# Optimization experiments

Hardware: AMD Instinct MI355X
Metric: run time of the kernel (lower is better)

## Reference

```python
import jax, jax.numpy as jnp
import numpy as np

B, N, D = 8, 9856, 256
HEADS = 8
WH, WW = 7, 11
HID = 512  # int(D * 2.0)
EPS = 1e-5


def layernorm(x, g, b):
    mu = jnp.mean(x, axis=-1, keepdims=True)
    var = jnp.mean(jnp.square(x - mu), axis=-1, keepdims=True)
    return (x - mu) * jax.lax.rsqrt(var + EPS) * g + b


def setup_inputs() -> dict:
    key = jax.random.key(0)
    ks = jax.random.split(key, 6)
    s = lambda k, shape: (jax.random.normal(k, shape, jnp.float32) * 0.02)
    return {
        "x": jax.random.normal(ks[0], (B, N, D), jnp.float32),
        "norm1_g": jnp.ones((D,), jnp.float32),
        "norm1_b": jnp.zeros((D,), jnp.float32),
        "in_proj_w": s(ks[1], (3 * D, D)),
        "in_proj_b": jnp.zeros((3 * D,), jnp.float32),
        "out_w": s(ks[2], (D, D)),
        "out_b": jnp.zeros((D,), jnp.float32),
        "norm2_g": jnp.ones((D,), jnp.float32),
        "norm2_b": jnp.zeros((D,), jnp.float32),
        "fc1_w": s(ks[3], (HID, D)),
        "fc1_b": jnp.zeros((HID,), jnp.float32),
        "fc2_w": s(ks[4], (D, HID)),
        "fc2_b": jnp.zeros((D,), jnp.float32),
        "h": 56,
        "w": 176,
    }


def reference(x, norm1_g, norm1_b, in_proj_w, in_proj_b, out_w, out_b,
              norm2_g, norm2_b, fc1_w, fc1_b, fc2_w, fc2_b, h, w):
    Bx, Nx, Dx = x.shape
    n_h, n_w = h // WH, w // WW  # chosen dims divide evenly -> pad_h = pad_w = 0
    hd = Dx // HEADS
    L = WH * WW  # 77 tokens per window

    res = x
    xn = layernorm(x, norm1_g, norm1_b)

    # window partition: (B, h*w, D) -> (B*n_h*n_w, wh*ww, D)
    win = xn.reshape(Bx, n_h, WH, n_w, WW, Dx)
    win = win.transpose(0, 1, 3, 2, 4, 5).reshape(-1, L, Dx)

    # MultiheadAttention (batch_first) on each window independently
    qkv = win @ in_proj_w.T + in_proj_b          # (NW, L, 3D)
    q, k, v = jnp.split(qkv, 3, axis=-1)
    NW = win.shape[0]
    q = q.reshape(NW, L, HEADS, hd).transpose(0, 2, 1, 3)
    k = k.reshape(NW, L, HEADS, hd).transpose(0, 2, 1, 3)
    v = v.reshape(NW, L, HEADS, hd).transpose(0, 2, 1, 3)
    scores = jnp.einsum("nhld,nhmd->nhlm", q, k) / jnp.sqrt(jnp.float32(hd))
    attn = jax.nn.softmax(scores, axis=-1)
    o = jnp.einsum("nhlm,nhmd->nhld", attn, v)   # (NW, H, L, hd)
    o = o.transpose(0, 2, 1, 3).reshape(NW, L, Dx)
    o = o @ out_w.T + out_b

    # window reverse: (B*n_h*n_w, wh*ww, D) -> (B, h*w, D)
    o = o.reshape(Bx, n_h, n_w, WH, WW, Dx)
    o = o.transpose(0, 1, 3, 2, 4, 5).reshape(Bx, Nx, Dx)

    x = res + o
    res = x
    xn2 = layernorm(x, norm2_g, norm2_b)
    hmid = jax.nn.gelu(xn2 @ fc1_w.T + fc1_b, approximate=False)
    mlp = hmid @ fc2_w.T + fc2_b
    return res + mlp
```

## Files before the change

### kernel.cpp

```cpp
#include <hip/hip_runtime.h>
#include <hip/hip_bf16.h>

typedef unsigned short u16;
typedef unsigned int   u32;

typedef __bf16 bf16x8 __attribute__((ext_vector_type(8)));
typedef float  f32x4  __attribute__((ext_vector_type(4)));

__device__ __forceinline__ u16 f2bf(float f) {
  u32 u = __float_as_uint(f);
  u += 0x7fffu + ((u >> 16) & 1u);
  return (u16)(u >> 16);
}
__device__ __forceinline__ u32 pack2(float a, float b) {
  return (u32)f2bf(a) | ((u32)f2bf(b) << 16);
}
__device__ __forceinline__ void gld16(const void* g, void* l) {
  __builtin_amdgcn_global_load_lds(
      (const __attribute__((address_space(1))) unsigned int*)g,
      (__attribute__((address_space(3))) unsigned int*)l, 16, 0, 0);
}

#define TOK_M   78848
#define DIM     256
#define NWIN    1024
#define WINL    77

template<int K, int NF>
__device__ __forceinline__ void cvt_chunk(const float* __restrict__ src,
                                          u16* __restrict__ dst, int rel)
{
  constexpr int KT = K / 32;
  constexpr int PN = NF * 16;
  const int lane  = rel & 63;
  const int g     = rel >> 6;
  const int nf    = g % NF;
  const int kt    = (g / NF) % KT;
  const int panel = g / (NF * KT);
  const int col   = panel * PN + nf * 16 + (lane & 15);
  const int k0    = kt * 32 + (lane >> 4) * 8;
  const float4 a = *(const float4*)(src + (size_t)col * K + k0);
  const float4 b = *(const float4*)(src + (size_t)col * K + k0 + 4);
  uint4 o;
  o.x = pack2(a.x, a.y); o.y = pack2(a.z, a.w);
  o.z = pack2(b.x, b.y); o.w = pack2(b.z, b.w);
  *(uint4*)(dst + (size_t)rel * 8) = o;
}
__device__ __forceinline__ void cvt_plain(const float* __restrict__ src,
                                          u16* __restrict__ dst, int rel)
{
  const int i = rel * 8;
  const float4 a = *(const float4*)(src + i);
  const float4 b = *(const float4*)(src + i + 4);
  uint4 o;
  o.x = pack2(a.x, a.y); o.y = pack2(a.z, a.w);
  o.z = pack2(b.x, b.y); o.w = pack2(b.z, b.w);
  *(uint4*)(dst + i) = o;
}

__global__ __launch_bounds__(256)
void cvt_w(const float* __restrict__ wqkv, const float* __restrict__ wout,
           const float* __restrict__ w1, const float* __restrict__ w2,
           u16* __restrict__ out)
{
  const int c = blockIdx.x * 256 + threadIdx.x;
  if      (c < 24576) cvt_chunk<256, 8>(wqkv, out,          c);
  else if (c < 32768) cvt_plain(wout, out + 196608, c - 24576);
  else if (c < 49152) cvt_chunk<256, 8>(w1,   out + 262144, c - 32768);
  else                cvt_plain(w2,   out + 393216, c - 49152);
}

template<int NPAN, int EPI, int OBF, int PERM>
__global__ __launch_bounds__(256, 2)
void lngemm(const float* __restrict__ X, const u16* __restrict__ Wimg,
            const float* __restrict__ lg, const float* __restrict__ lb,
            const float* __restrict__ bias, void* __restrict__ Cout)
{
  constexpr int K  = 256;
  constexpr int KT = K / 32;
  constexpr int N  = NPAN * 128;
  constexpr int NSTEP = NPAN * KT;
  __shared__ u16 At[64 * K];
  __shared__ u16 Bs[4][4096];

  const int tid  = threadIdx.x;
  const int wave = tid >> 6, lane = tid & 63;
  const int quad = lane >> 4, l16 = lane & 15;
  const int wy = wave >> 1, wx = wave & 1;
  const int rowbase = blockIdx.x * 64;

  {
    const float4 gg = *(const float4*)(lg + lane * 4);
    const float4 bb = *(const float4*)(lb + lane * 4);
    const int c = lane * 4;
    float4 xv[16];
#pragma unroll
    for (int r = 0; r < 16; ++r)
      xv[r] = *(const float4*)(X + (size_t)(rowbase + wave * 16 + r) * 256 + c);
#pragma unroll
    for (int r = 0; r < 16; ++r) {
      const int row = wave * 16 + r;
      const float4 v = xv[r];
      float s = v.x + v.y + v.z + v.w;
#pragma unroll
      for (int off = 32; off; off >>= 1) s += __shfl_xor(s, off);
      const float mu = s * (1.f / 256.f);
      const float dx = v.x - mu, dy = v.y - mu, dz = v.z - mu, dw = v.w - mu;
      float q = dx * dx + dy * dy + dz * dz + dw * dw;
#pragma unroll
      for (int off = 32; off; off >>= 1) q += __shfl_xor(q, off);
      const float rstd = rsqrtf(q * (1.f / 256.f) + 1e-5f);
      uint2 o;
      o.x = pack2(dx * rstd * gg.x + bb.x, dy * rstd * gg.y + bb.y);
      o.y = pack2(dz * rstd * gg.z + bb.z, dw * rstd * gg.w + bb.w);
      *(uint2*)(At + row * 256 + (c ^ ((row & 7) * 8))) = o;
    }
  }
  gld16(Wimg + tid * 8,        Bs[0] + tid * 8);
  gld16(Wimg + 2048 + tid * 8, Bs[0] + 2048 + tid * 8);
  gld16(Wimg + 4096 + tid * 8,        Bs[1] + tid * 8);
  gld16(Wimg + 4096 + 2048 + tid * 8, Bs[1] + 2048 + tid * 8);

  int step = 0;
  for (int np = 0; np < NPAN; ++np) {
    f32x4 acc[2][4];
#pragma unroll
    for (int mi = 0; mi < 2; ++mi)
#pragma unroll
      for (int ni = 0; ni < 4; ++ni) {
        f32x4 z = {0.f, 0.f, 0.f, 0.f};
        acc[mi][ni] = z;
      }
#pragma unroll
    for (int kt = 0; kt < KT; ++kt, ++step) {
      {
        const int sn = (step + 2 < NSTEP) ? step + 2 : NSTEP - 1;
        const u16* src = Wimg + (size_t)sn * 4096;
        u16* dst = Bs[(step + 2) & 3];
        gld16(src + tid * 8,        dst + tid * 8);
        gld16(src + 2048 + tid * 8, dst + 2048 + tid * 8);
      }
      asm volatile("s_waitcnt vmcnt(4) lgkmcnt(0)" ::: "memory");
      __builtin_amdgcn_s_barrier();
      __builtin_amdgcn_sched_barrier(0);
      bf16x8 af[2], bv[4];
#pragma unroll
      for (int mi = 0; mi < 2; ++mi) {
        const int row = wy * 32 + mi * 16 + l16;
        af[mi] = *(const bf16x8*)(At + row * 256 +
                                  ((kt * 32 + quad * 8) ^ ((row & 7) * 8)));
      }
#pragma unroll
      for (int ni = 0; ni < 4; ++ni)
        bv[ni] = *(const bf16x8*)(Bs[step & 3] + ((wx * 4 + ni) * 64 + lane) * 8);
#pragma unroll
      for (int mi = 0; mi < 2; ++mi)
#pragma unroll
        for (int ni = 0; ni < 4; ++ni)
          acc[mi][ni] = __builtin_amdgcn_mfma_f32_16x16x32_bf16(
              af[mi], bv[ni], acc[mi][ni], 0, 0, 0);
    }
    const int col0 = np * 128 + wx * 64 + l16;
#pragma unroll
    for (int mi = 0; mi < 2; ++mi) {
      const int r = rowbase + wy * 32 + mi * 16 + quad * 4;
#pragma unroll
      for (int e = 0; e < 4; ++e) {
        const int gr = r + e;
        size_t orow = (size_t)gr;
        if (PERM) {
          const int b  = gr / 9856, n = gr - b * 9856;
          const int y  = n / 176,  xc = n - y * 176;
          const int ih = y / 7,    rr = y - ih * 7;
          const int iw = xc / 11,  cc = xc - iw * 11;
          orow = (size_t)(((b * 8 + ih) * 16 + iw)) * 77 + rr * 11 + cc;
        }
#pragma unroll
        for (int ni = 0; ni < 4; ++ni) {
          const int col = col0 + ni * 16;
          float v = acc[mi][ni][e] + bias[col];
          if (EPI == 2) v = 0.5f * v * (1.f + erff(v * 0.70710678118654752f));
          const size_t idx = orow * N + col;
          if (OBF) ((u16*)Cout)[idx] = f2bf(v);
          else     ((float*)Cout)[idx] = v;
        }
      }
    }
  }
}

template<int EPI, int OBF>
__global__ __launch_bounds__(256, 2)
void gemm_mfma(const u16* __restrict__ A, const u16* __restrict__ W,
               const float* __restrict__ bias, const float* res,
               void* Cout, int N, int K)
{
  __shared__ u16 As[4][4096];
  __shared__ u16 Bs[4][4096];

  const int tid  = threadIdx.x;
  const int wave = tid >> 6, lane = tid & 63;
  const int wy = wave >> 1, wx = wave & 1;
  const int quad = lane >> 4, l16 = lane & 15;
  const int m0 = blockIdx.y * 128;
  const int n0 = blockIdx.x * 128;

  const int s0 = tid, s1 = tid + 256;
  const int r0 = s0 >> 2, r1 = s1 >> 2;
  const int kb0 = (s0 & 3) ^ ((r0 >> 1) & 3);
  const int kb1 = (s1 & 3) ^ ((r1 >> 1) & 3);
  const u16* Ag0 = A + (size_t)(m0 + r0) * K + kb0 * 8;
  const u16* Ag1 = A + (size_t)(m0 + r1) * K + kb1 * 8;
  const u16* Bg0 = W + (size_t)(n0 + r0) * K + kb0 * 8;
  const u16* Bg1 = W + (size_t)(n0 + r1) * K + kb1 * 8;

  const int kbs = quad ^ ((l16 >> 1) & 3);
  const int aoff = (wy * 64 + l16) * 32 + kbs * 8;
  const int boff = (wx * 64 + l16) * 32 + kbs * 8;

  f32x4 acc[4][4];
#pragma unroll
  for (int i = 0; i < 4; ++i)
#pragma unroll
    for (int j = 0; j < 4; ++j) {
      f32x4 z = {0.f, 0.f, 0.f, 0.f};
      acc[i][j] = z;
    }

  const int NT = K >> 5;
  auto stage = [&](int tile, int buf) {
    const int ko = tile * 32;
    gld16(Ag0 + ko, &As[buf][s0 * 8]);
    gld16(Ag1 + ko, &As[buf][s1 * 8]);
    gld16(Bg0 + ko, &Bs[buf][s0 * 8]);
    gld16(Bg1 + ko, &Bs[buf][s1 * 8]);
  };
  stage(0, 0);
  stage(1, 1);

  for (int t = 0; t < NT; ++t) {
    stage((t + 2 < NT) ? t + 2 : NT - 1, (t + 2) & 3);
    asm volatile("s_waitcnt vmcnt(8) lgkmcnt(0)" ::: "memory");
    __builtin_amdgcn_s_barrier();
    __builtin_amdgcn_sched_barrier(0);
    const u16* Ar = &As[t & 3][aoff];
    const u16* Br = &Bs[t & 3][boff];
    bf16x8 af[4], bv[4];
#pragma unroll
    for (int i = 0; i < 4; ++i) {
      af[i] = *(const bf16x8*)(Ar + i * 16 * 32);
      bv[i] = *(const bf16x8*)(Br + i * 16 * 32);
    }
#pragma unroll
    for (int mi = 0; mi < 4; ++mi)
#pragma unroll
      for (int ni = 0; ni < 4; ++ni)
        acc[mi][ni] = __builtin_amdgcn_mfma_f32_16x16x32_bf16(
            af[mi], bv[ni], acc[mi][ni], 0, 0, 0);
  }

  const int gr0 = m0 + wy * 64 + quad * 4;
  const int gc0 = n0 + wx * 64 + l16;
#pragma unroll
  for (int ni = 0; ni < 4; ++ni) {
    const int gc = gc0 + ni * 16;
    const float bvs = bias[gc];
#pragma unroll
    for (int mi = 0; mi < 4; ++mi) {
      const int gr = gr0 + mi * 16;
      f32x4 a = acc[mi][ni];
#pragma unroll
      for (int e = 0; e < 4; ++e) {
        float v = a[e] + bvs;
        const size_t idx = (size_t)(gr + e) * N + gc;
        if (EPI == 1) v += res[idx];
        else if (EPI == 2) v = 0.5f * v * (1.f + erff(v * 0.70710678118654752f));
        if (OBF) ((u16*)Cout)[idx] = f2bf(v);
        else     ((float*)Cout)[idx] = v;
      }
    }
  }
}

#define PSTR 104
__global__ __launch_bounds__(128)
void attn_mfma(const u16* __restrict__ qkv, u16* __restrict__ onat)
{
  __shared__ __bf16 Pb[2][80 * PSTR];

  const int tid  = threadIdx.x;
  const int wave = tid >> 6, lane = tid & 63;
  const int quad = lane >> 4, l16 = lane & 15;
  const int pair = blockIdx.x * 2 + wave;
  const int nw   = pair >> 3, head = pair & 7;
  const size_t base = (size_t)nw * 77 * 768;
  const int hoff = head * 32;
  __bf16* P = Pb[wave];

  {
    uint4 z = {0, 0, 0, 0};
    for (int r = lane; r < 80; r += 64) {
      *(uint4*)(P + r * PSTR + 80) = z;
      *(uint4*)(P + r * PSTR + 88) = z;
    }
  }

  bf16x8 qf[5], kf[5];
  const u16* qp = qkv + base + hoff + quad * 8;
#pragma unroll
  for (int mi = 0; mi < 5; ++mi) {
    const size_t row = (size_t)(l16 + 16 * mi) * 768;
    qf[mi] = *(const bf16x8*)(qp + row);
    kf[mi] = *(const bf16x8*)(qp + row + 256);
  }

  f32x4 s[5][5];
#pragma unroll
  for (int mi = 0; mi < 5; ++mi)
#pragma unroll
    for (int ni = 0; ni < 5; ++ni) {
      f32x4 z = {0.f, 0.f, 0.f, 0.f};
      s[mi][ni] = z;
    }
#pragma unroll
  for (int mi = 0; mi < 5; ++mi)
#pragma unroll
    for (int ni = 0; ni < 5; ++ni)
      s[mi][ni] = __builtin_amdgcn_mfma_f32_16x16x32_bf16(
          qf[mi], kf[ni], s[mi][ni], 0, 0, 0);

  bf16x8 vf[3][2];
  {
    const __bf16* vbb = (const __bf16*)(qkv + base + 512 + hoff + l16);
#pragma unroll
    for (int ks = 0; ks < 3; ++ks)
#pragma unroll
      for (int ni = 0; ni < 2; ++ni)
#pragma unroll
        for (int jj = 0; jj < 8; ++jj) {
          const int k = ks * 32 + quad * 8 + jj;
          vf[ks][ni][jj] = (k < 77) ? vbb[(size_t)k * 768 + 16 * ni] : (__bf16)0.f;
        }
  }

  if (l16 >= 13) {
#pragma unroll
    for (int mi = 0; mi < 5; ++mi)
#pragma unroll
      for (int e = 0; e < 4; ++e) s[mi][4][e] = -1e30f;
  }

  const float c = 0.17677669529663687f * 1.4426950408889634f;
  float inv[5][4];
#pragma unroll
  for (int mi = 0; mi < 5; ++mi)
#pragma unroll
    for (int e = 0; e < 4; ++e) {
      float mx = s[mi][0][e];
#pragma unroll
      for (int ni = 1; ni < 5; ++ni) mx = fmaxf(mx, s[mi][ni][e]);
#pragma unroll
      for (int off = 1; off < 16; off <<= 1) mx = fmaxf(mx, __shfl_xor(mx, off));
      float sum = 0.f;
#pragma unroll
      for (int ni = 0; ni < 5; ++ni) {
        const float ev = exp2f((s[mi][ni][e] - mx) * c);
        s[mi][ni][e] = ev;
        sum += ev;
      }
#pragma unroll
      for (int off = 1; off < 16; off <<= 1) sum += __shfl_xor(sum, off);
      inv[mi][e] = 1.f / sum;
    }

#pragma unroll
  for (int mi = 0; mi < 5; ++mi)
#pragma unroll
    for (int e = 0; e < 4; ++e) {
      const int m = quad * 4 + e + 16 * mi;
#pragma unroll
      for (int ni = 0; ni < 5; ++ni)
        P[m * PSTR + l16 + 16 * ni] = (__bf16)(s[mi][ni][e] * inv[mi][e]);
    }

  f32x4 o[5][2];
#pragma unroll
  for (int mi = 0; mi < 5; ++mi)
#pragma unroll
    for (int ni = 0; ni < 2; ++ni) {
      f32x4 z = {0.f, 0.f, 0.f, 0.f};
      o[mi][ni] = z;
    }
#pragma unroll
  for (int ks = 0; ks < 3; ++ks)
#pragma unroll
    for (int mi = 0; mi < 5; ++mi) {
      const bf16x8 af = *(const bf16x8*)(P + (l16 + 16 * mi) * PSTR + ks * 32 + quad * 8);
#pragma unroll
      for (int ni = 0; ni < 2; ++ni)
        o[mi][ni] = __builtin_amdgcn_mfma_f32_16x16x32_bf16(
            af, vf[ks][ni], o[mi][ni], 0, 0, 0);
    }

  const int b  = nw >> 7;
  const int ih = (nw >> 4) & 7;
  const int iw = nw & 15;
#pragma unroll
  for (int mi = 0; mi < 5; ++mi)
#pragma unroll
    for (int e = 0; e < 4; ++e) {
      const int t = quad * 4 + e + 16 * mi;
      if (t < 77) {
        const int rr = t / 11, cc = t - rr * 11;
        const int y = ih * 7 + rr, xc = iw * 11 + cc;
        const size_t nat = (size_t)b * 9856 + (size_t)y * 176 + xc;
        u16* dst = onat + nat * DIM + hoff + l16;
        dst[0]  = f2bf(o[mi][0][e]);
        dst[16] = f2bf(o[mi][1][e]);
      }
    }
}

extern "C" void kernel_launch(void* const* d_in, const int* in_sizes, int n_in,
                              void* d_out, int out_size, void* d_ws, size_t ws_size,
                              hipStream_t stream)
{
  (void)in_sizes; (void)n_in; (void)out_size; (void)ws_size;
  const float* x    = (const float*)d_in[0];
  const float* g1   = (const float*)d_in[1];
  const float* b1   = (const float*)d_in[2];
  const float* wqkv = (const float*)d_in[3];
  const float* bqkv = (const float*)d_in[4];
  const float* wout = (const float*)d_in[5];
  const float* bout = (const float*)d_in[6];
  const float* g2   = (const float*)d_in[7];
  const float* b2   = (const float*)d_in[8];
  const float* w1   = (const float*)d_in[9];
  const float* bf1  = (const float*)d_in[10];
  const float* w2   = (const float*)d_in[11];
  const float* bf2  = (const float*)d_in[12];

  char* ws = (char*)d_ws;
  u16*   qkv  = (u16*)(ws);
  u16*   onat = (u16*)(ws + 161480704);
  u16*   wb   = (u16*)(ws + 201850880);
  u16*   wqkv_b = wb;
  u16*   wout_b = wb + 196608;
  u16*   w1_b   = wb + 262144;
  u16*   w2_b   = wb + 393216;
  float* x2   = (float*)d_out;

  cvt_w<<<256, 256, 0, stream>>>(wqkv, wout, w1, w2, wb);
  lngemm<6, 0, 1, 1><<<1232, 256, 0, stream>>>(x, wqkv_b, g1, b1, bqkv, qkv);
  attn_mfma<<<4096, 128, 0, stream>>>(qkv, onat);
  gemm_mfma<1, 0><<<dim3(2, 616), 256, 0, stream>>>(onat, wout_b, bout, x, x2, 256, 256);
  lngemm<4, 2, 1, 0><<<1232, 256, 0, stream>>>(x2, w1_b, g2, b2, bf1, qkv);
  gemm_mfma<1, 0><<<dim3(2, 616), 256, 0, stream>>>(qkv, w2_b, bf2, x2, x2, 256, 512);
}
```

Measured before the change: 582.0 us.

## Fuse out-proj with residual+LN2, keep A fragments in registers across GEMMs

Replaces the generic 128x128 tiled GEMM with row-panel GEMMs that hold each wave's A fragments in registers and stream pre-swizzled weight panels through LDS. The out-projection kernel now also adds the residual and computes LayerNorm2, writing both x2 and a bf16 normalized copy. This removes the separate reread of x2 in the LN-fused fc1 kernel. The QKV kernel reuses one LDS buffer for both the A tile and the B stages, raising occupancy to 3 blocks. Holding A in registers increases register pressure, and per-wave 16-row tiles lower weight reuse per block.

Result: faster. 510.4 us (-12.3%).

```diff
diff --git a/kernel.cpp b/kernel.cpp
--- a/kernel.cpp
+++ b/kernel.cpp
@@ -23,8 +23,6 @@
 
 #define TOK_M   78848
 #define DIM     256
-#define NWIN    1024
-#define WINL    77
 
 template<int K, int NF>
 __device__ __forceinline__ void cvt_chunk(const float* __restrict__ src,
@@ -46,17 +44,6 @@
   o.z = pack2(b.x, b.y); o.w = pack2(b.z, b.w);
   *(uint4*)(dst + (size_t)rel * 8) = o;
 }
-__device__ __forceinline__ void cvt_plain(const float* __restrict__ src,
-                                          u16* __restrict__ dst, int rel)
-{
-  const int i = rel * 8;
-  const float4 a = *(const float4*)(src + i);
-  const float4 b = *(const float4*)(src + i + 4);
-  uint4 o;
-  o.x = pack2(a.x, a.y); o.y = pack2(a.z, a.w);
-  o.z = pack2(b.x, b.y); o.w = pack2(b.z, b.w);
-  *(uint4*)(dst + i) = o;
-}
 
 __global__ __launch_bounds__(256)
 void cvt_w(const float* __restrict__ wqkv, const float* __restrict__ wout,
@@ -65,23 +52,21 @@
 {
   const int c = blockIdx.x * 256 + threadIdx.x;
   if      (c < 24576) cvt_chunk<256, 8>(wqkv, out,          c);
-  else if (c < 32768) cvt_plain(wout, out + 196608, c - 24576);
+  else if (c < 32768) cvt_chunk<256, 8>(wout, out + 196608, c - 24576);
   else if (c < 49152) cvt_chunk<256, 8>(w1,   out + 262144, c - 32768);
-  else                cvt_plain(w2,   out + 393216, c - 49152);
-}
-
-template<int NPAN, int EPI, int OBF, int PERM>
-__global__ __launch_bounds__(256, 2)
-void lngemm(const float* __restrict__ X, const u16* __restrict__ Wimg,
-            const float* __restrict__ lg, const float* __restrict__ lb,
-            const float* __restrict__ bias, void* __restrict__ Cout)
-{
-  constexpr int K  = 256;
-  constexpr int KT = K / 32;
+  else                cvt_chunk<512, 8>(w2,   out + 393216, c - 49152);
+}
+
+template<int NPAN>
+__global__ __launch_bounds__(256, 3)
+void lngemm_qkv(const float* __restrict__ X, const u16* __restrict__ Wimg,
+                const float* __restrict__ lg, const float* __restrict__ lb,
+                const float* __restrict__ bias, u16* __restrict__ Cout)
+{
+  constexpr int KT = 8;
   constexpr int N  = NPAN * 128;
   constexpr int NSTEP = NPAN * KT;
-  __shared__ u16 At[64 * K];
-  __shared__ u16 Bs[4][4096];
+  __shared__ u16 U[16384];
 
   const int tid  = threadIdx.x;
   const int wave = tid >> 6, lane = tid & 63;
@@ -113,13 +98,25 @@
       uint2 o;
       o.x = pack2(dx * rstd * gg.x + bb.x, dy * rstd * gg.y + bb.y);
       o.y = pack2(dz * rstd * gg.z + bb.z, dw * rstd * gg.w + bb.w);
-      *(uint2*)(At + row * 256 + (c ^ ((row & 7) * 8))) = o;
-    }
-  }
-  gld16(Wimg + tid * 8,        Bs[0] + tid * 8);
-  gld16(Wimg + 2048 + tid * 8, Bs[0] + 2048 + tid * 8);
-  gld16(Wimg + 4096 + tid * 8,        Bs[1] + tid * 8);
-  gld16(Wimg + 4096 + 2048 + tid * 8, Bs[1] + 2048 + tid * 8);
+      *(uint2*)(U + row * 256 + (c ^ ((row & 7) * 8))) = o;
+    }
+  }
+  __syncthreads();
+  bf16x8 af[2][8];
+#pragma unroll
+  for (int mi = 0; mi < 2; ++mi) {
+    const int row = wy * 32 + mi * 16 + l16;
+#pragma unroll
+    for (int kt = 0; kt < 8; ++kt)
+      af[mi][kt] = *(const bf16x8*)(U + row * 256 +
+                                    ((kt * 32 + quad * 8) ^ ((row & 7) * 8)));
+  }
+  __syncthreads();
+
+  gld16(Wimg + tid * 8,               U + tid * 8);
+  gld16(Wimg + 2048 + tid * 8,        U + 2048 + tid * 8);
+  gld16(Wimg + 4096 + tid * 8,        U + 4096 + tid * 8);
+  gld16(Wimg + 4096 + 2048 + tid * 8, U + 4096 + 2048 + tid * 8);
 
   int step = 0;
   for (int np = 0; np < NPAN; ++np) {
@@ -131,6 +128,87 @@
         f32x4 z = {0.f, 0.f, 0.f, 0.f};
         acc[mi][ni] = z;
       }
+#pragma unroll
+    for (int kt = 0; kt < KT; ++kt, ++step) {
+      {
+        const int sn = (step + 2 < NSTEP) ? step + 2 : NSTEP - 1;
+        const u16* src = Wimg + (size_t)sn * 4096;
+        u16* dst = U + ((step + 2) & 3) * 4096;
+        gld16(src + tid * 8,        dst + tid * 8);
+        gld16(src + 2048 + tid * 8, dst + 2048 + tid * 8);
+      }
+      asm volatile("s_waitcnt vmcnt(4) lgkmcnt(0)" ::: "memory");
+      __builtin_amdgcn_s_barrier();
+      __builtin_amdgcn_sched_barrier(0);
+      const u16* B0 = U + (step & 3) * 4096;
+      bf16x8 bv[4];
+#pragma unroll
+      for (int ni = 0; ni < 4; ++ni)
+        bv[ni] = *(const bf16x8*)(B0 + ((wx * 4 + ni) * 64 + lane) * 8);
+#pragma unroll
+      for (int mi = 0; mi < 2; ++mi)
+#pragma unroll
+        for (int ni = 0; ni < 4; ++ni)
+          acc[mi][ni] = __builtin_amdgcn_mfma_f32_16x16x32_bf16(
+              af[mi][kt], bv[ni], acc[mi][ni], 0, 0, 0);
+    }
+    const int col0 = np * 128 + wx * 64 + l16;
+#pragma unroll
+    for (int mi = 0; mi < 2; ++mi) {
+      const int r = rowbase + wy * 32 + mi * 16 + quad * 4;
+#pragma unroll
+      for (int e = 0; e < 4; ++e) {
+        const int gr = r + e;
+        const int b  = gr / 9856, n = gr - b * 9856;
+        const int y  = n / 176,  xc = n - y * 176;
+        const int ih = y / 7,    rr = y - ih * 7;
+        const int iw = xc / 11,  cc = xc - iw * 11;
+        const size_t orow = (size_t)(((b * 8 + ih) * 16 + iw)) * 77 + rr * 11 + cc;
+#pragma unroll
+        for (int ni = 0; ni < 4; ++ni) {
+          const int col = col0 + ni * 16;
+          Cout[orow * N + col] = f2bf(acc[mi][ni][e] + bias[col]);
+        }
+      }
+    }
+  }
+}
+
+template<int K, int NPAN, int EPI, int OBF>
+__global__ __launch_bounds__(256, 3)
+void gemmA(const u16* __restrict__ A, const u16* __restrict__ Wimg,
+           const float* __restrict__ bias, const float* __restrict__ res,
+           void* __restrict__ Cout)
+{
+  constexpr int KT = K / 32;
+  constexpr int N  = NPAN * 128;
+  constexpr int NSTEP = NPAN * KT;
+  __shared__ u16 Bs[4][4096];
+
+  const int tid  = threadIdx.x;
+  const int wave = tid >> 6, lane = tid & 63;
+  const int quad = lane >> 4, l16 = lane & 15;
+  const int row0 = blockIdx.x * 64 + wave * 16;
+
+  bf16x8 af[KT];
+  {
+    const u16* Ap = A + (size_t)(row0 + l16) * K + quad * 8;
+#pragma unroll
+    for (int kt = 0; kt < KT; ++kt) af[kt] = *(const bf16x8*)(Ap + kt * 32);
+  }
+  gld16(Wimg + tid * 8,               Bs[0] + tid * 8);
+  gld16(Wimg + 2048 + tid * 8,        Bs[0] + 2048 + tid * 8);
+  gld16(Wimg + 4096 + tid * 8,        Bs[1] + tid * 8);
+  gld16(Wimg + 4096 + 2048 + tid * 8, Bs[1] + 2048 + tid * 8);
+
+  int step = 0;
+  for (int np = 0; np < NPAN; ++np) {
+    f32x4 acc[8];
+#pragma unroll
+    for (int nf = 0; nf < 8; ++nf) {
+      f32x4 z = {0.f, 0.f, 0.f, 0.f};
+      acc[nf] = z;
+    }
 #pragma unroll
     for (int kt = 0; kt < KT; ++kt, ++step) {
       {
@@ -143,141 +221,121 @@
       asm volatile("s_waitcnt vmcnt(4) lgkmcnt(0)" ::: "memory");
       __builtin_amdgcn_s_barrier();
       __builtin_amdgcn_sched_barrier(0);
-      bf16x8 af[2], bv[4];
-#pragma unroll
-      for (int mi = 0; mi < 2; ++mi) {
-        const int row = wy * 32 + mi * 16 + l16;
-        af[mi] = *(const bf16x8*)(At + row * 256 +
-                                  ((kt * 32 + quad * 8) ^ ((row & 7) * 8)));
-      }
-#pragma unroll
-      for (int ni = 0; ni < 4; ++ni)
-        bv[ni] = *(const bf16x8*)(Bs[step & 3] + ((wx * 4 + ni) * 64 + lane) * 8);
-#pragma unroll
-      for (int mi = 0; mi < 2; ++mi)
-#pragma unroll
-        for (int ni = 0; ni < 4; ++ni)
-          acc[mi][ni] = __builtin_amdgcn_mfma_f32_16x16x32_bf16(
-              af[mi], bv[ni], acc[mi][ni], 0, 0, 0);
-    }
-    const int col0 = np * 128 + wx * 64 + l16;
-#pragma unroll
-    for (int mi = 0; mi < 2; ++mi) {
-      const int r = rowbase + wy * 32 + mi * 16 + quad * 4;
+      const u16* B0 = Bs[step & 3];
+#pragma unroll
+      for (int nf = 0; nf < 8; ++nf) {
+        const bf16x8 bv = *(const bf16x8*)(B0 + (nf * 64 + lane) * 8);
+        acc[nf] = __builtin_amdgcn_mfma_f32_16x16x32_bf16(
+            af[kt], bv, acc[nf], 0, 0, 0);
+      }
+    }
+#pragma unroll
+    for (int nf = 0; nf < 8; ++nf) {
+      const int col = np * 128 + nf * 16 + l16;
+      const float bvs = bias[col];
 #pragma unroll
       for (int e = 0; e < 4; ++e) {
-        const int gr = r + e;
-        size_t orow = (size_t)gr;
-        if (PERM) {
-          const int b  = gr / 9856, n = gr - b * 9856;
-          const int y  = n / 176,  xc = n - y * 176;
-          const int ih = y / 7,    rr = y - ih * 7;
-          const int iw = xc / 11,  cc = xc - iw * 11;
-          orow = (size_t)(((b * 8 + ih) * 16 + iw)) * 77 + rr * 11 + cc;
-        }
-#pragma unroll
-        for (int ni = 0; ni < 4; ++ni) {
-          const int col = col0 + ni * 16;
-          float v = acc[mi][ni][e] + bias[col];
-          if (EPI == 2) v = 0.5f * v * (1.f + erff(v * 0.70710678118654752f));
-          const size_t idx = orow * N + col;
-          if (OBF) ((u16*)Cout)[idx] = f2bf(v);
-          else     ((float*)Cout)[idx] = v;
-        }
-      }
-    }
-  }
-}
-
-template<int EPI, int OBF>
-__global__ __launch_bounds__(256, 2)
-void gemm_mfma(const u16* __restrict__ A, const u16* __restrict__ W,
-               const float* __restrict__ bias, const float* res,
-               void* Cout, int N, int K)
-{
-  __shared__ u16 As[4][4096];
-  __shared__ u16 Bs[4][4096];
-
-  const int tid  = threadIdx.x;
-  const int wave = tid >> 6, lane = tid & 63;
-  const int wy = wave >> 1, wx = wave & 1;
-  const int quad = lane >> 4, l16 = lane & 15;
-  const int m0 = blockIdx.y * 128;
-  const int n0 = blockIdx.x * 128;
-
-  const int s0 = tid, s1 = tid + 256;
-  const int r0 = s0 >> 2, r1 = s1 >> 2;
-  const int kb0 = (s0 & 3) ^ ((r0 >> 1) & 3);
-  const int kb1 = (s1 & 3) ^ ((r1 >> 1) & 3);
-  const u16* Ag0 = A + (size_t)(m0 + r0) * K + kb0 * 8;
-  const u16* Ag1 = A + (size_t)(m0 + r1) * K + kb1 * 8;
-  const u16* Bg0 = W + (size_t)(n0 + r0) * K + kb0 * 8;
-  const u16* Bg1 = W + (size_t)(n0 + r1) * K + kb1 * 8;
-
-  const int kbs = quad ^ ((l16 >> 1) & 3);
-  const int aoff = (wy * 64 + l16) * 32 + kbs * 8;
-  const int boff = (wx * 64 + l16) * 32 + kbs * 8;
-
-  f32x4 acc[4][4];
-#pragma unroll
-  for (int i = 0; i < 4; ++i)
-#pragma unroll
-    for (int j = 0; j < 4; ++j) {
-      f32x4 z = {0.f, 0.f, 0.f, 0.f};
-      acc[i][j] = z;
-    }
-
-  const int NT = K >> 5;
-  auto stage = [&](int tile, int buf) {
-    const int ko = tile * 32;
-    gld16(Ag0 + ko, &As[buf][s0 * 8]);
-    gld16(Ag1 + ko, &As[buf][s1 * 8]);
-    gld16(Bg0 + ko, &Bs[buf][s0 * 8]);
-    gld16(Bg1 + ko, &Bs[buf][s1 * 8]);
-  };
-  stage(0, 0);
-  stage(1, 1);
-
-  for (int t = 0; t < NT; ++t) {
-    stage((t + 2 < NT) ? t + 2 : NT - 1, (t + 2) & 3);
-    asm volatile("s_waitcnt vmcnt(8) lgkmcnt(0)" ::: "memory");
-    __builtin_amdgcn_s_barrier();
-    __builtin_amdgcn_sched_barrier(0);
-    const u16* Ar = &As[t & 3][aoff];
-    const u16* Br = &Bs[t & 3][boff];
-    bf16x8 af[4], bv[4];
-#pragma unroll
-    for (int i = 0; i < 4; ++i) {
-      af[i] = *(const bf16x8*)(Ar + i * 16 * 32);
-      bv[i] = *(const bf16x8*)(Br + i * 16 * 32);
-    }
-#pragma unroll
-    for (int mi = 0; mi < 4; ++mi)
-#pragma unroll
-      for (int ni = 0; ni < 4; ++ni)
-        acc[mi][ni] = __builtin_amdgcn_mfma_f32_16x16x32_bf16(
-            af[mi], bv[ni], acc[mi][ni], 0, 0, 0);
-  }
-
-  const int gr0 = m0 + wy * 64 + quad * 4;
-  const int gc0 = n0 + wx * 64 + l16;
-#pragma unroll
-  for (int ni = 0; ni < 4; ++ni) {
-    const int gc = gc0 + ni * 16;
-    const float bvs = bias[gc];
-#pragma unroll
-    for (int mi = 0; mi < 4; ++mi) {
-      const int gr = gr0 + mi * 16;
-      f32x4 a = acc[mi][ni];
-#pragma unroll
-      for (int e = 0; e < 4; ++e) {
-        float v = a[e] + bvs;
-        const size_t idx = (size_t)(gr + e) * N + gc;
+        const int row = row0 + quad * 4 + e;
+        const size_t idx = (size_t)row * N + col;
+        float v = acc[nf][e] + bvs;
         if (EPI == 1) v += res[idx];
         else if (EPI == 2) v = 0.5f * v * (1.f + erff(v * 0.70710678118654752f));
         if (OBF) ((u16*)Cout)[idx] = f2bf(v);
         else     ((float*)Cout)[idx] = v;
       }
+    }
+  }
+}
+
+__global__ __launch_bounds__(256, 3)
+void gemmA_ln(const u16* __restrict__ A, const u16* __restrict__ Wimg,
+              const float* __restrict__ bias, const float* __restrict__ res,
+              float* __restrict__ x2, const float* __restrict__ g2,
+              const float* __restrict__ b2, u16* __restrict__ xn2)
+{
+  constexpr int NSTEP = 16;
+  __shared__ u16 Bs[4][4096];
+
+  const int tid  = threadIdx.x;
+  const int wave = tid >> 6, lane = tid & 63;
+  const int quad = lane >> 4, l16 = lane & 15;
+  const int row0 = blockIdx.x * 64 + wave * 16;
+
+  bf16x8 af[8];
+  {
+    const u16* Ap = A + (size_t)(row0 + l16) * 256 + quad * 8;
+#pragma unroll
+    for (int kt = 0; kt < 8; ++kt) af[kt] = *(const bf16x8*)(Ap + kt * 32);
+  }
+  gld16(Wimg + tid * 8,               Bs[0] + tid * 8);
+  gld16(Wimg + 2048 + tid * 8,        Bs[0] + 2048 + tid * 8);
+  gld16(Wimg + 4096 + tid * 8,        Bs[1] + tid * 8);
+  gld16(Wimg + 4096 + 2048 + tid * 8, Bs[1] + 2048 + tid * 8);
+
+  f32x4 acc[2][8];
+#pragma unroll
+  for (int np = 0; np < 2; ++np)
+#pragma unroll
+    for (int nf = 0; nf < 8; ++nf) {
+      f32x4 z = {0.f, 0.f, 0.f, 0.f};
+      acc[np][nf] = z;
+    }
+#pragma unroll
+  for (int step = 0; step < NSTEP; ++step) {
+    const int np = step >> 3, kt = step & 7;
+    {
+      const int sn = (step + 2 < NSTEP) ? step + 2 : NSTEP - 1;
+      const u16* src = Wimg + (size_t)sn * 4096;
+      u16* dst = Bs[(step + 2) & 3];
+      gld16(src + tid * 8,        dst + tid * 8);
+      gld16(src + 2048 + tid * 8, dst + 2048 + tid * 8);
+    }
+    asm volatile("s_waitcnt vmcnt(4) lgkmcnt(0)" ::: "memory");
+    __builtin_amdgcn_s_barrier();
+    __builtin_amdgcn_sched_barrier(0);
+    const u16* B0 = Bs[step & 3];
+#pragma unroll
+    for (int nf = 0; nf < 8; ++nf) {
+      const bf16x8 bv = *(const bf16x8*)(B0 + (nf * 64 + lane) * 8);
+      acc[np][nf] = __builtin_amdgcn_mfma_f32_16x16x32_bf16(
+          af[kt], bv, acc[np][nf], 0, 0, 0);
+    }
+  }
+
+  float gg[16], bbv[16], bsv[16];
+#pragma unroll
+  for (int i = 0; i < 16; ++i) {
+    const int col = (i >> 3) * 128 + (i & 7) * 16 + l16;
+    gg[i] = g2[col]; bbv[i] = b2[col]; bsv[i] = bias[col];
+  }
+#pragma unroll
+  for (int e = 0; e < 4; ++e) {
+    const int row = row0 + quad * 4 + e;
+    const float* rp = res + (size_t)row * 256;
+    float v[16];
+    float s = 0.f;
+#pragma unroll
+    for (int i = 0; i < 16; ++i) {
+      const int col = (i >> 3) * 128 + (i & 7) * 16 + l16;
+      v[i] = acc[i >> 3][i & 7][e] + bsv[i] + rp[col];
+      s += v[i];
+    }
+#pragma unroll
+    for (int off = 1; off < 16; off <<= 1) s += __shfl_xor(s, off);
+    const float mu = s * (1.f / 256.f);
+    float q = 0.f;
+#pragma unroll
+    for (int i = 0; i < 16; ++i) { const float d = v[i] - mu; q += d * d; }
+#pragma unroll
+    for (int off = 1; off < 16; off <<= 1) q += __shfl_xor(q, off);
+    const float rstd = rsqrtf(q * (1.f / 256.f) + 1e-5f);
+    float* xp = x2 + (size_t)row * 256;
+    u16*   yp = xn2 + (size_t)row * 256;
+#pragma unroll
+    for (int i = 0; i < 16; ++i) {
+      const int col = (i >> 3) * 128 + (i & 7) * 16 + l16;
+      xp[col] = v[i];
+      yp[col] = f2bf((v[i] - mu) * rstd * gg[i] + bbv[i]);
     }
   }
 }
@@ -442,18 +500,20 @@
 
   char* ws = (char*)d_ws;
   u16*   qkv  = (u16*)(ws);
+  u16*   xn2  = (u16*)(ws + 121110528);
   u16*   onat = (u16*)(ws + 161480704);
   u16*   wb   = (u16*)(ws + 201850880);
   u16*   wqkv_b = wb;
   u16*   wout_b = wb + 196608;
   u16*   w1_b   = wb + 262144;
   u16*   w2_b   = wb + 393216;
+  u16*   h    = qkv;
   float* x2   = (float*)d_out;
 
   cvt_w<<<256, 256, 0, stream>>>(wqkv, wout, w1, w2, wb);
-  lngemm<6, 0, 1, 1><<<1232, 256, 0, stream>>>(x, wqkv_b, g1, b1, bqkv, qkv);
+  lngemm_qkv<6><<<1232, 256, 0, stream>>>(x, wqkv_b, g1, b1, bqkv, qkv);
   attn_mfma<<<4096, 128, 0, stream>>>(qkv, onat);
-  gemm_mfma<1, 0><<<dim3(2, 616), 256, 0, stream>>>(onat, wout_b, bout, x, x2, 256, 256);
-  lngemm<4, 2, 1, 0><<<1232, 256, 0, stream>>>(x2, w1_b, g2, b2, bf1, qkv);
-  gemm_mfma<1, 0><<<dim3(2, 616), 256, 0, stream>>>(qkv, w2_b, bf2, x2, x2, 256, 512);
-}
+  gemmA_ln<<<1232, 256, 0, stream>>>(onat, wout_b, bout, x, x2, g2, b2, xn2);
+  gemmA<256, 4, 2, 1><<<1232, 256, 0, stream>>>(xn2, w1_b, bf1, nullptr, h);
+  gemmA<512, 2, 1, 0><<<1232, 256, 0, stream>>>(h, w2_b, bf2, x2, x2);
+}
```
